# Kernel tuning notes

Measured on AMD Instinct MI355X. Metric: run time of the kernel, lower is better.

## Reference

```python
import jax, jax.numpy as jnp
import numpy as np

N_NODES = 100000

def setup_inputs() -> dict:
    key = jax.random.key(0)
    k = jax.random.split(key, 6)
    N, E, D = N_NODES, 1600000, 128
    x = jax.random.normal(k[0], (N, D), dtype=jnp.float32)
    edge_src = jax.random.randint(k[1], (E,), 0, N, dtype=jnp.int32)
    edge_dst = jax.random.randint(k[2], (E,), 0, N, dtype=jnp.int32)
    edge_weight = jax.random.uniform(k[3], (E,), dtype=jnp.float32)
    W1 = jax.random.normal(k[4], (D, D), dtype=jnp.float32) * (1.0 / np.sqrt(D))
    W2 = jax.random.normal(k[5], (D, D), dtype=jnp.float32) * (1.0 / np.sqrt(D))
    return {"x": x, "edge_src": edge_src, "edge_dst": edge_dst,
            "edge_weight": edge_weight, "W1": W1, "W2": W2}

def _graph_conv(x, W, src, dst, ew, n_nodes):
    # GraphConv: h = A @ (x @ W); A given as weighted edge list.
    h = x @ W                               # [N, D_out]
    msg = h[src] * ew[:, None]              # [E, D_out] gather + scale
    return jax.ops.segment_sum(msg, dst, num_segments=n_nodes)  # [N, D_out]

def reference(x, edge_src, edge_dst, edge_weight, W1, W2):
    n = x.shape[0]
    # layer 1: tanh(GraphConv) ; Dropout(0) is identity
    x = jnp.tanh(_graph_conv(x, W1, edge_src, edge_dst, edge_weight, n))
    # layer 2
    x = jnp.tanh(_graph_conv(x, W2, edge_src, edge_dst, edge_weight, n))
    return x
```

## Files before the change

kernel.cpp:

```cpp
#include <hip/hip_runtime.h>
#include <hip/hip_bf16.h>

#define N_NODES 100000
#define N_EDGES 1600000
#define D 128
#define BSZ 128
#define NBUCK 782
#define EPW 8192
#define NWG1 ((N_EDGES + EPW - 1) / EPW)
#define CAP 4096
#define OTS 272

typedef unsigned int  uint4n  __attribute__((ext_vector_type(4)));
typedef float         float4n __attribute__((ext_vector_type(4)));
typedef _Float16      half8n  __attribute__((ext_vector_type(8)));
typedef _Float16      half4n  __attribute__((ext_vector_type(4)));

#define SWZ(row, kb) (((row) << 8) + ((kb) ^ (((row) & 15) << 4)))

__device__ __forceinline__ float fast_tanh(float x) {
    float t = __builtin_amdgcn_exp2f(x * 2.885390081777927f);
    return 1.0f - 2.0f * __builtin_amdgcn_rcpf(t + 1.0f);
}

__global__ __launch_bounds__(256) void k_wprep(const float* __restrict__ W1,
                                               const float* __restrict__ W2,
                                               char* __restrict__ Wt,
                                               int* __restrict__ bcnt) {
    if (blockIdx.x == 32) {
        for (int i = threadIdx.x; i < NBUCK; i += 256) bcnt[i] = 0;
        return;
    }
    const float* W = (blockIdx.x < 16) ? W1 : W2;
    char* dst = Wt + ((blockIdx.x < 16) ? 0 : 32768);
    int t = (blockIdx.x & 15) * 256 + threadIdx.x;
    int idx = t * 4;
    int k = idx >> 7, c = idx & 127;
    float4 wv = *(const float4*)&W[idx];
    *(_Float16*)(dst + SWZ(c + 0, k * 2)) = (_Float16)wv.x;
    *(_Float16*)(dst + SWZ(c + 1, k * 2)) = (_Float16)wv.y;
    *(_Float16*)(dst + SWZ(c + 2, k * 2)) = (_Float16)wv.z;
    *(_Float16*)(dst + SWZ(c + 3, k * 2)) = (_Float16)wv.w;
}


__global__ __launch_bounds__(256) void k_hist1(const int* __restrict__ dst,
                                               int* __restrict__ bcnt) {
    __shared__ int h[NBUCK];
    for (int i = threadIdx.x; i < NBUCK; i += 256) h[i] = 0;
    __syncthreads();
    int base = blockIdx.x * EPW;
    int end  = min(base + EPW, N_EDGES);
    for (int i = base + threadIdx.x; i < end; i += 256)
        atomicAdd(&h[dst[i] >> 7], 1);
    __syncthreads();
    for (int i = threadIdx.x; i < NBUCK; i += 256)
        if (h[i]) atomicAdd(&bcnt[i], h[i]);
}

__global__ void k_scanN(const int* __restrict__ bcnt, int* __restrict__ boff,
                        int* __restrict__ gcur) {
    __shared__ int tmp[256];
    int tid = threadIdx.x;
    int carry = 0;
    for (int c = 0; c < (NBUCK + 255) / 256; c++) {
        int i = c * 256 + tid;
        int v = (i < NBUCK) ? bcnt[i] : 0;
        tmp[tid] = v;
        __syncthreads();
        int run = v;
        for (int off = 1; off < 256; off <<= 1) {
            int t = (tid >= off) ? tmp[tid - off] : 0;
            __syncthreads();
            run += t;
            tmp[tid] = run;
            __syncthreads();
        }
        int excl = carry + run - v;
        if (i < NBUCK) { boff[i] = excl; gcur[i] = excl; }
        int tot = tmp[255];
        __syncthreads();
        carry += tot;
    }
    if (tid == 0) boff[NBUCK] = N_EDGES;
}

__global__ __launch_bounds__(256) void k_scat1(const int* __restrict__ src,
                                               const int* __restrict__ dst,
                                               const float* __restrict__ ew,
                                               int* __restrict__ gcur,
                                               int2* __restrict__ ebuf) {
    __shared__ int h[NBUCK];
    __shared__ int rb[NBUCK];
    for (int i = threadIdx.x; i < NBUCK; i += 256) h[i] = 0;
    __syncthreads();
    int base = blockIdx.x * EPW;
    int end  = min(base + EPW, N_EDGES);
    for (int i = base + threadIdx.x; i < end; i += 256)
        atomicAdd(&h[dst[i] >> 7], 1);
    __syncthreads();
    for (int i = threadIdx.x; i < NBUCK; i += 256) {
        int c = h[i];
        if (c) rb[i] = atomicAdd(&gcur[i], c);
    }
    __syncthreads();
    for (int i = base + threadIdx.x; i < end; i += 256) {
        int d  = dst[i];
        int bk = d >> 7;
        int p  = atomicAdd(&rb[bk], 1);
        ebuf[p] = make_int2((src[i] << 8) | (d & 127), __float_as_int(ew[i]));
    }
}

__global__ __launch_bounds__(512) void k_sortb(int2* __restrict__ ebuf,
                                               const int* __restrict__ boff,
                                               int* __restrict__ rowptr) {
    __shared__ int2 se[CAP];
    __shared__ int cnt[BSZ];
    __shared__ int cur[BSZ];
    int tid = threadIdx.x;
    int b   = blockIdx.x;
    int e0 = boff[b], e1 = boff[b + 1];
    int m  = e1 - e0;
    if (tid < BSZ) cnt[tid] = 0;
    __syncthreads();
    int2 ovf;
    bool hasOvf = false;
    for (int i = tid; i < m; i += 512) {
        int2 v = ebuf[e0 + i];
        if (i < CAP) se[i] = v;
        else { ovf = v; hasOvf = true; }
        atomicAdd(&cnt[v.x & (BSZ - 1)], 1);
    }
    __syncthreads();
    if (tid < 64) {
        int a  = cnt[tid * 2], bq = cnt[tid * 2 + 1];
        int s  = a + bq;
        int incl = s;
        #pragma unroll
        for (int off = 1; off < 64; off <<= 1) {
            int t = __shfl_up(incl, off, 64);
            if (tid >= off) incl += t;
        }
        int ex = incl - s;
        cur[tid * 2]     = ex;
        cur[tid * 2 + 1] = ex + a;
        int node = b * BSZ + tid * 2;
        if (node     <= N_NODES) rowptr[node]     = e0 + ex;
        if (node + 1 <= N_NODES) rowptr[node + 1] = e0 + ex + a;
    }
    __syncthreads();
    for (int i = tid; i < m && i < CAP; i += 512) {
        int2 v = se[i];
        int p = atomicAdd(&cur[v.x & (BSZ - 1)], 1);
        ebuf[e0 + p] = v;
    }
    if (hasOvf) {
        int p = atomicAdd(&cur[ovf.x & (BSZ - 1)], 1);
        ebuf[e0 + p] = ovf;
    }
}

template<bool XF16>
__global__ __launch_bounds__(256) void k_gemm(const void* __restrict__ Xv,
                                              const char* __restrict__ Wt,
                                              _Float16* __restrict__ H, int n) {
    __shared__ char smem[17408];
    char* sA = smem;
    int tid  = threadIdx.x;
    int lane = tid & 63, w = tid >> 6;
    int rows0 = blockIdx.x * 64;

    int rb = (w >> 1) * 32;
    int cb = (w & 1) * 64;
    int lr = lane & 15;
    int kg = (lane >> 4) * 16;

    float4n acc[2][4] = {};

    if (XF16) {
        const _Float16* Xh = (const _Float16*)Xv;
        const _Float16* Arow0 = Xh + (size_t)(rows0 + rb + lr) * 128 + (kg >> 1);
        #pragma unroll
        for (int ks = 0; ks < 4; ks++) {
            half8n bwk[4];
            #pragma unroll
            for (int ct = 0; ct < 4; ct++)
                bwk[ct] = *(const half8n*)(Wt + SWZ(cb + ct * 16 + lr, ks * 64 + kg));
            half8n af[2];
            #pragma unroll
            for (int rt = 0; rt < 2; rt++)
                af[rt] = *(const half8n*)(Arow0 + (size_t)rt * 16 * 128 + ks * 32);
            #pragma unroll
            for (int rt = 0; rt < 2; rt++)
                #pragma unroll
                for (int ct = 0; ct < 4; ct++)
                    acc[rt][ct] = __builtin_amdgcn_mfma_f32_16x16x32_f16(af[rt], bwk[ct], acc[rt][ct], 0, 0, 0);
        }
    } else {
        const float* Xf = (const float*)Xv;
        #pragma unroll
        for (int rep = 0; rep < 8; rep++) {
            int ef = rep * 1024 + tid * 4;
            int r = ef >> 7, c = ef & 127;
            int rg = rows0 + r;
            float4 xv = make_float4(0.f, 0.f, 0.f, 0.f);
            if (rg < n) xv = *(const float4*)(Xf + (size_t)rg * 128 + c);
            half4n hv;
            hv[0] = (_Float16)xv.x; hv[1] = (_Float16)xv.y;
            hv[2] = (_Float16)xv.z; hv[3] = (_Float16)xv.w;
            *(half4n*)(sA + SWZ(r, c * 2)) = hv;
        }
        __syncthreads();
        #pragma unroll
        for (int ks = 0; ks < 4; ks++) {
            half8n bwk[4];
            #pragma unroll
            for (int ct = 0; ct < 4; ct++)
                bwk[ct] = *(const half8n*)(Wt + SWZ(cb + ct * 16 + lr, ks * 64 + kg));
            half8n af[2];
            #pragma unroll
            for (int rt = 0; rt < 2; rt++)
                af[rt] = *(const half8n*)(sA + SWZ(rb + rt * 16 + lr, ks * 64 + kg));
            #pragma unroll
            for (int rt = 0; rt < 2; rt++)
                #pragma unroll
                for (int ct = 0; ct < 4; ct++)
                    acc[rt][ct] = __builtin_amdgcn_mfma_f32_16x16x32_f16(af[rt], bwk[ct], acc[rt][ct], 0, 0, 0);
        }
        __syncthreads();
    }

    char* OT = smem;
    int rloc = rb + (lane >> 4) * 4;
    #pragma unroll
    for (int rt = 0; rt < 2; rt++) {
        #pragma unroll
        for (int ct = 0; ct < 4; ct++) {
            int col = cb + ct * 16 + lr;
            #pragma unroll
            for (int r = 0; r < 4; r++)
                *(_Float16*)(OT + (rloc + rt * 16 + r) * OTS + col * 2) = (_Float16)acc[rt][ct][r];
        }
    }
    __syncthreads();
    #pragma unroll
    for (int rep = 0; rep < 4; rep++) {
        int ef = rep * 2048 + tid * 8;
        int r = ef >> 7, c = ef & 127;
        int rg = rows0 + r;
        if (rg < n) {
            half8n v = *(const half8n*)(OT + r * OTS + c * 2);
            *(half8n*)&H[(size_t)rg * 128 + c] = v;
        }
    }
}

template<bool OUTF16>
__global__ __launch_bounds__(256) void k_agg(const _Float16* __restrict__ H,
                                             const int* __restrict__ rowptr,
                                             const int2* __restrict__ ebuf,
                                             void* __restrict__ outv, int n) {
    int wv   = (blockIdx.x * 256 + threadIdx.x) >> 6;
    int lane = threadIdx.x & 63;
    int g = lane >> 4;
    int c = lane & 15;
    int node = wv * 4 + g;
    if (node >= n) return;
    const char* Hc = (const char*)H + (c << 4);
    int e0 = rowptr[node], e1 = rowptr[node + 1];
    float acc[8] = {};
    int e = e0;
    for (; e + 4 <= e1; e += 4) {
        int2 d0 = ebuf[e];
        int2 d1 = ebuf[e + 1];
        int2 d2 = ebuf[e + 2];
        int2 d3 = ebuf[e + 3];
        half8n v0 = *(const half8n*)(Hc + (size_t)((unsigned)d0.x & 0xFFFFFF00u));
        half8n v1 = *(const half8n*)(Hc + (size_t)((unsigned)d1.x & 0xFFFFFF00u));
        half8n v2 = *(const half8n*)(Hc + (size_t)((unsigned)d2.x & 0xFFFFFF00u));
        half8n v3 = *(const half8n*)(Hc + (size_t)((unsigned)d3.x & 0xFFFFFF00u));
        float w0 = __int_as_float(d0.y);
        float w1 = __int_as_float(d1.y);
        float w2 = __int_as_float(d2.y);
        float w3 = __int_as_float(d3.y);
        #pragma unroll
        for (int j = 0; j < 8; j++) acc[j] = __builtin_fmaf((float)v0[j], w0, acc[j]);
        #pragma unroll
        for (int j = 0; j < 8; j++) acc[j] = __builtin_fmaf((float)v1[j], w1, acc[j]);
        #pragma unroll
        for (int j = 0; j < 8; j++) acc[j] = __builtin_fmaf((float)v2[j], w2, acc[j]);
        #pragma unroll
        for (int j = 0; j < 8; j++) acc[j] = __builtin_fmaf((float)v3[j], w3, acc[j]);
    }
    for (; e < e1; ++e) {
        int2 ed = ebuf[e];
        half8n v = *(const half8n*)(Hc + (size_t)((unsigned)ed.x & 0xFFFFFF00u));
        float w = __int_as_float(ed.y);
        #pragma unroll
        for (int j = 0; j < 8; j++) acc[j] = __builtin_fmaf((float)v[j], w, acc[j]);
    }
    if (OUTF16) {
        half8n hv;
        #pragma unroll
        for (int j = 0; j < 8; j++) hv[j] = (_Float16)fast_tanh(acc[j]);
        *(uint4n*)((_Float16*)outv + (size_t)node * 128 + c * 8) = *(uint4n*)&hv;
    } else {
        float* op = (float*)outv + (size_t)node * 128 + c * 8;
        float4n o0, o1;
        o0.x = fast_tanh(acc[0]); o0.y = fast_tanh(acc[1]);
        o0.z = fast_tanh(acc[2]); o0.w = fast_tanh(acc[3]);
        o1.x = fast_tanh(acc[4]); o1.y = fast_tanh(acc[5]);
        o1.z = fast_tanh(acc[6]); o1.w = fast_tanh(acc[7]);
        __builtin_nontemporal_store(o0, (float4n*)op);
        __builtin_nontemporal_store(o1, (float4n*)(op + 4));
    }
}


extern "C" void kernel_launch(void* const* d_in, const int* in_sizes, int n_in,
                              void* d_out, int out_size, void* d_ws, size_t ws_size,
                              hipStream_t stream) {
    const float* x    = (const float*)d_in[0];
    const int*   esrc = (const int*)d_in[1];
    const int*   edst = (const int*)d_in[2];
    const float* ew   = (const float*)d_in[3];
    const float* W1   = (const float*)d_in[4];
    const float* W2   = (const float*)d_in[5];
    float* out = (float*)d_out;

    _Float16* hbuf = (_Float16*)d_ws;
    _Float16* act1 = hbuf + (size_t)N_NODES * D;
    int2* ebuf     = (int2*)(act1 + (size_t)N_NODES * D);
    int*  bcnt     = (int*)(ebuf + N_EDGES);
    int*  boff     = bcnt + NBUCK;
    int*  gcur     = boff + (NBUCK + 1);
    int*  rowptr   = gcur + NBUCK;
    char* Wt       = (char*)(rowptr + N_NODES + 8);
    (void)ws_size; (void)in_sizes; (void)n_in; (void)out_size;

    k_wprep<<<33, 256, 0, stream>>>(W1, W2, Wt, bcnt);
    k_hist1<<<NWG1, 256, 0, stream>>>(edst, bcnt);
    k_scanN<<<1, 256, 0, stream>>>(bcnt, boff, gcur);
    k_scat1<<<NWG1, 256, 0, stream>>>(esrc, edst, ew, gcur, ebuf);
    k_sortb<<<NBUCK, 512, 0, stream>>>(ebuf, boff, rowptr);

    int gemm_blocks = (N_NODES + 63) / 64;
    int agg_blocks  = (N_NODES + 15) / 16;

    k_gemm<false><<<gemm_blocks, 256, 0, stream>>>(x, Wt, hbuf, N_NODES);
    k_agg<true><<<agg_blocks, 256, 0, stream>>>(hbuf, rowptr, ebuf, act1, N_NODES);
    k_gemm<true><<<gemm_blocks, 256, 0, stream>>>(act1, Wt + 32768, hbuf, N_NODES);
    k_agg<false><<<agg_blocks, 256, 0, stream>>>(hbuf, rowptr, ebuf, out, N_NODES);
}
```

Baseline: 230.5 us.

## Merge preprocessing kernels and co-schedule edge scatter with first GEMM

Weight prep and the edge histogram now run as one launch, with the bucket counter cleared by a memset. The edge bucket scatter and the first-layer GEMM run as independent block ranges of one kernel, so the GEMM overlaps the CSR build. The second GEMM now stages its fp16 input in shared memory instead of reading A fragments straight from global memory. This removes launch gaps and idle tails between small kernels, at the cost of a mixed kernel whose shared-memory and register footprint is the larger of the two roles.

```diff
diff --git a/kernel.cpp b/kernel.cpp
--- a/kernel.cpp
+++ b/kernel.cpp
@@ -23,33 +23,29 @@
     return 1.0f - 2.0f * __builtin_amdgcn_rcpf(t + 1.0f);
 }
 
-__global__ __launch_bounds__(256) void k_wprep(const float* __restrict__ W1,
-                                               const float* __restrict__ W2,
-                                               char* __restrict__ Wt,
-                                               int* __restrict__ bcnt) {
-    if (blockIdx.x == 32) {
-        for (int i = threadIdx.x; i < NBUCK; i += 256) bcnt[i] = 0;
+__global__ __launch_bounds__(256) void k_wprep_hist(const float* __restrict__ W1,
+                                                    const float* __restrict__ W2,
+                                                    char* __restrict__ Wt,
+                                                    const int* __restrict__ dst,
+                                                    int* __restrict__ bcnt) {
+    if (blockIdx.x < 32) {
+        const float* W = (blockIdx.x < 16) ? W1 : W2;
+        char* dstp = Wt + ((blockIdx.x < 16) ? 0 : 32768);
+        int t = (blockIdx.x & 15) * 256 + threadIdx.x;
+        int idx = t * 4;
+        int k = idx >> 7, c = idx & 127;
+        float4 wv = *(const float4*)&W[idx];
+        *(_Float16*)(dstp + SWZ(c + 0, k * 2)) = (_Float16)wv.x;
+        *(_Float16*)(dstp + SWZ(c + 1, k * 2)) = (_Float16)wv.y;
+        *(_Float16*)(dstp + SWZ(c + 2, k * 2)) = (_Float16)wv.z;
+        *(_Float16*)(dstp + SWZ(c + 3, k * 2)) = (_Float16)wv.w;
         return;
     }
-    const float* W = (blockIdx.x < 16) ? W1 : W2;
-    char* dst = Wt + ((blockIdx.x < 16) ? 0 : 32768);
-    int t = (blockIdx.x & 15) * 256 + threadIdx.x;
-    int idx = t * 4;
-    int k = idx >> 7, c = idx & 127;
-    float4 wv = *(const float4*)&W[idx];
-    *(_Float16*)(dst + SWZ(c + 0, k * 2)) = (_Float16)wv.x;
-    *(_Float16*)(dst + SWZ(c + 1, k * 2)) = (_Float16)wv.y;
-    *(_Float16*)(dst + SWZ(c + 2, k * 2)) = (_Float16)wv.z;
-    *(_Float16*)(dst + SWZ(c + 3, k * 2)) = (_Float16)wv.w;
-}
-
-
-__global__ __launch_bounds__(256) void k_hist1(const int* __restrict__ dst,
-                                               int* __restrict__ bcnt) {
     __shared__ int h[NBUCK];
     for (int i = threadIdx.x; i < NBUCK; i += 256) h[i] = 0;
     __syncthreads();
-    int base = blockIdx.x * EPW;
+    int hb   = blockIdx.x - 32;
+    int base = hb * EPW;
     int end  = min(base + EPW, N_EDGES);
     for (int i = base + threadIdx.x; i < end; i += 256)
         atomicAdd(&h[dst[i] >> 7], 1);
@@ -85,30 +81,105 @@
     if (tid == 0) boff[NBUCK] = N_EDGES;
 }
 
-__global__ __launch_bounds__(256) void k_scat1(const int* __restrict__ src,
-                                               const int* __restrict__ dst,
-                                               const float* __restrict__ ew,
-                                               int* __restrict__ gcur,
-                                               int2* __restrict__ ebuf) {
-    __shared__ int h[NBUCK];
-    __shared__ int rb[NBUCK];
-    for (int i = threadIdx.x; i < NBUCK; i += 256) h[i] = 0;
-    __syncthreads();
-    int base = blockIdx.x * EPW;
-    int end  = min(base + EPW, N_EDGES);
-    for (int i = base + threadIdx.x; i < end; i += 256)
-        atomicAdd(&h[dst[i] >> 7], 1);
-    __syncthreads();
-    for (int i = threadIdx.x; i < NBUCK; i += 256) {
-        int c = h[i];
-        if (c) rb[i] = atomicAdd(&gcur[i], c);
-    }
-    __syncthreads();
-    for (int i = base + threadIdx.x; i < end; i += 256) {
-        int d  = dst[i];
-        int bk = d >> 7;
-        int p  = atomicAdd(&rb[bk], 1);
-        ebuf[p] = make_int2((src[i] << 8) | (d & 127), __float_as_int(ew[i]));
+__global__ __launch_bounds__(256) void k_scat_gemm(const int* __restrict__ src,
+                                                   const int* __restrict__ dst,
+                                                   const float* __restrict__ ew,
+                                                   int* __restrict__ gcur,
+                                                   int2* __restrict__ ebuf,
+                                                   const float* __restrict__ Xf,
+                                                   const char* __restrict__ Wt,
+                                                   _Float16* __restrict__ H, int n) {
+    __shared__ char smem[17408];
+    int tid = threadIdx.x;
+
+    if (blockIdx.x < NWG1) {
+        int* h  = (int*)smem;
+        int* rb = h + NBUCK;
+        for (int i = tid; i < NBUCK; i += 256) h[i] = 0;
+        __syncthreads();
+        int base = blockIdx.x * EPW;
+        int end  = min(base + EPW, N_EDGES);
+        for (int i = base + tid; i < end; i += 256)
+            atomicAdd(&h[dst[i] >> 7], 1);
+        __syncthreads();
+        for (int i = tid; i < NBUCK; i += 256) {
+            int c = h[i];
+            if (c) rb[i] = atomicAdd(&gcur[i], c);
+        }
+        __syncthreads();
+        for (int i = base + tid; i < end; i += 256) {
+            int d  = dst[i];
+            int bk = d >> 7;
+            int p  = atomicAdd(&rb[bk], 1);
+            ebuf[p] = make_int2((src[i] << 8) | (d & 127), __float_as_int(ew[i]));
+        }
+        return;
+    }
+
+    char* sA = smem;
+    int lane = tid & 63, w = tid >> 6;
+    int rows0 = (blockIdx.x - NWG1) * 64;
+
+    int rb2 = (w >> 1) * 32;
+    int cb = (w & 1) * 64;
+    int lr = lane & 15;
+    int kg = (lane >> 4) * 16;
+
+    #pragma unroll
+    for (int rep = 0; rep < 8; rep++) {
+        int ef = rep * 1024 + tid * 4;
+        int r = ef >> 7, c = ef & 127;
+        int rg = rows0 + r;
+        float4 xv = make_float4(0.f, 0.f, 0.f, 0.f);
+        if (rg < n) xv = *(const float4*)(Xf + (size_t)rg * 128 + c);
+        half4n hv;
+        hv[0] = (_Float16)xv.x; hv[1] = (_Float16)xv.y;
+        hv[2] = (_Float16)xv.z; hv[3] = (_Float16)xv.w;
+        *(half4n*)(sA + SWZ(r, c * 2)) = hv;
+    }
+    __syncthreads();
+
+    float4n acc[2][4] = {};
+    #pragma unroll
+    for (int ks = 0; ks < 4; ks++) {
+        half8n bwk[4];
+        #pragma unroll
+        for (int ct = 0; ct < 4; ct++)
+            bwk[ct] = *(const half8n*)(Wt + SWZ(cb + ct * 16 + lr, ks * 64 + kg));
+        half8n af[2];
+        #pragma unroll
+        for (int rt = 0; rt < 2; rt++)
+            af[rt] = *(const half8n*)(sA + SWZ(rb2 + rt * 16 + lr, ks * 64 + kg));
+        #pragma unroll
+        for (int rt = 0; rt < 2; rt++)
+            #pragma unroll
+            for (int ct = 0; ct < 4; ct++)
+                acc[rt][ct] = __builtin_amdgcn_mfma_f32_16x16x32_f16(af[rt], bwk[ct], acc[rt][ct], 0, 0, 0);
+    }
+
+    __syncthreads();
+    char* OT = smem;
+    int rloc = rb2 + (lane >> 4) * 4;
+    #pragma unroll
+    for (int rt = 0; rt < 2; rt++) {
+        #pragma unroll
+        for (int ct = 0; ct < 4; ct++) {
+            int col = cb + ct * 16 + lr;
+            #pragma unroll
+            for (int r = 0; r < 4; r++)
+                *(_Float16*)(OT + (rloc + rt * 16 + r) * OTS + col * 2) = (_Float16)acc[rt][ct][r];
+        }
+    }
+    __syncthreads();
+    #pragma unroll
+    for (int rep = 0; rep < 4; rep++) {
+        int ef = rep * 2048 + tid * 8;
+        int r = ef >> 7, c = ef & 127;
+        int rg = rows0 + r;
+        if (rg < n) {
+            half8n v = *(const half8n*)(OT + r * OTS + c * 2);
+            *(half8n*)&H[(size_t)rg * 128 + c] = v;
+        }
     }
 }
 
@@ -161,10 +232,9 @@
     }
 }
 
-template<bool XF16>
-__global__ __launch_bounds__(256) void k_gemm(const void* __restrict__ Xv,
-                                              const char* __restrict__ Wt,
-                                              _Float16* __restrict__ H, int n) {
+__global__ __launch_bounds__(256) void k_gemm2(const _Float16* __restrict__ Xh,
+                                               const char* __restrict__ Wt,
+                                               _Float16* __restrict__ H, int n) {
     __shared__ char smem[17408];
     char* sA = smem;
     int tid  = threadIdx.x;
@@ -176,61 +246,36 @@
     int lr = lane & 15;
     int kg = (lane >> 4) * 16;
 
+    #pragma unroll
+    for (int rep = 0; rep < 4; rep++) {
+        int ef = rep * 2048 + tid * 8;
+        int r = ef >> 7, c = ef & 127;
+        int rg = rows0 + r;
+        half8n v = half8n(0);
+        if (rg < n) v = *(const half8n*)(Xh + (size_t)rg * 128 + c);
+        *(half8n*)(sA + SWZ(r, c * 2)) = v;
+    }
+    __syncthreads();
+
     float4n acc[2][4] = {};
-
-    if (XF16) {
-        const _Float16* Xh = (const _Float16*)Xv;
-        const _Float16* Arow0 = Xh + (size_t)(rows0 + rb + lr) * 128 + (kg >> 1);
-        #pragma unroll
-        for (int ks = 0; ks < 4; ks++) {
-            half8n bwk[4];
+    #pragma unroll
+    for (int ks = 0; ks < 4; ks++) {
+        half8n bwk[4];
+        #pragma unroll
+        for (int ct = 0; ct < 4; ct++)
+            bwk[ct] = *(const half8n*)(Wt + SWZ(cb + ct * 16 + lr, ks * 64 + kg));
+        half8n af[2];
+        #pragma unroll
+        for (int rt = 0; rt < 2; rt++)
+            af[rt] = *(const half8n*)(sA + SWZ(rb + rt * 16 + lr, ks * 64 + kg));
+        #pragma unroll
+        for (int rt = 0; rt < 2; rt++)
             #pragma unroll
             for (int ct = 0; ct < 4; ct++)
-                bwk[ct] = *(const half8n*)(Wt + SWZ(cb + ct * 16 + lr, ks * 64 + kg));
-            half8n af[2];
-            #pragma unroll
-            for (int rt = 0; rt < 2; rt++)
-                af[rt] = *(const half8n*)(Arow0 + (size_t)rt * 16 * 128 + ks * 32);
-            #pragma unroll
-            for (int rt = 0; rt < 2; rt++)
-                #pragma unroll
-                for (int ct = 0; ct < 4; ct++)
-                    acc[rt][ct] = __builtin_amdgcn_mfma_f32_16x16x32_f16(af[rt], bwk[ct], acc[rt][ct], 0, 0, 0);
-        }
-    } else {
-        const float* Xf = (const float*)Xv;
-        #pragma unroll
-        for (int rep = 0; rep < 8; rep++) {
-            int ef = rep * 1024 + tid * 4;
-            int r = ef >> 7, c = ef & 127;
-            int rg = rows0 + r;
-            float4 xv = make_float4(0.f, 0.f, 0.f, 0.f);
-            if (rg < n) xv = *(const float4*)(Xf + (size_t)rg * 128 + c);
-            half4n hv;
-            hv[0] = (_Float16)xv.x; hv[1] = (_Float16)xv.y;
-            hv[2] = (_Float16)xv.z; hv[3] = (_Float16)xv.w;
-            *(half4n*)(sA + SWZ(r, c * 2)) = hv;
-        }
-        __syncthreads();
-        #pragma unroll
-        for (int ks = 0; ks < 4; ks++) {
-            half8n bwk[4];
-            #pragma unroll
-            for (int ct = 0; ct < 4; ct++)
-                bwk[ct] = *(const half8n*)(Wt + SWZ(cb + ct * 16 + lr, ks * 64 + kg));
-            half8n af[2];
-            #pragma unroll
-            for (int rt = 0; rt < 2; rt++)
-                af[rt] = *(const half8n*)(sA + SWZ(rb + rt * 16 + lr, ks * 64 + kg));
-            #pragma unroll
-            for (int rt = 0; rt < 2; rt++)
-                #pragma unroll
-                for (int ct = 0; ct < 4; ct++)
-                    acc[rt][ct] = __builtin_amdgcn_mfma_f32_16x16x32_f16(af[rt], bwk[ct], acc[rt][ct], 0, 0, 0);
-        }
-        __syncthreads();
-    }
-
+                acc[rt][ct] = __builtin_amdgcn_mfma_f32_16x16x32_f16(af[rt], bwk[ct], acc[rt][ct], 0, 0, 0);
+    }
+
+    __syncthreads();
     char* OT = smem;
     int rloc = rb + (lane >> 4) * 4;
     #pragma unroll
@@ -339,17 +384,17 @@
     char* Wt       = (char*)(rowptr + N_NODES + 8);
     (void)ws_size; (void)in_sizes; (void)n_in; (void)out_size;
 
-    k_wprep<<<33, 256, 0, stream>>>(W1, W2, Wt, bcnt);
-    k_hist1<<<NWG1, 256, 0, stream>>>(edst, bcnt);
-    k_scanN<<<1, 256, 0, stream>>>(bcnt, boff, gcur);
-    k_scat1<<<NWG1, 256, 0, stream>>>(esrc, edst, ew, gcur, ebuf);
-    k_sortb<<<NBUCK, 512, 0, stream>>>(ebuf, boff, rowptr);
-
     int gemm_blocks = (N_NODES + 63) / 64;
     int agg_blocks  = (N_NODES + 15) / 16;
 
-    k_gemm<false><<<gemm_blocks, 256, 0, stream>>>(x, Wt, hbuf, N_NODES);
+    hipMemsetAsync(bcnt, 0, NBUCK * sizeof(int), stream);
+    k_wprep_hist<<<32 + NWG1, 256, 0, stream>>>(W1, W2, Wt, edst, bcnt);
+    k_scanN<<<1, 256, 0, stream>>>(bcnt, boff, gcur);
+    k_scat_gemm<<<NWG1 + gemm_blocks, 256, 0, stream>>>(esrc, edst, ew, gcur, ebuf,
+                                                        x, Wt, hbuf, N_NODES);
+    k_sortb<<<NBUCK, 512, 0, stream>>>(ebuf, boff, rowptr);
+
     k_agg<true><<<agg_blocks, 256, 0, stream>>>(hbuf, rowptr, ebuf, act1, N_NODES);
-    k_gemm<true><<<gemm_blocks, 256, 0, stream>>>(act1, Wt + 32768, hbuf, N_NODES);
+    k_gemm2<<<gemm_blocks, 256, 0, stream>>>(act1, Wt + 32768, hbuf, N_NODES);
     k_agg<false><<<agg_blocks, 256, 0, stream>>>(hbuf, rowptr, ebuf, out, N_NODES);
 }
```

Measured after the change: 222.5 us. 1.04x faster.
